# Performance work log

Measured on AMD Instinct MI355X. Metric: run time of the kernel, lower is better.

## Reference

```python
import jax, jax.numpy as jnp
import numpy as np

HEADS = 8
DIM_HEAD = 64
MAX_POS = 512
SCALE = DIM_HEAD ** -0.5

def setup_inputs() -> dict:
    key = jax.random.key(0)
    ks = jax.random.split(key, 4)
    b, n, dim = 32, 512, 512
    x = jax.random.normal(ks[0], (b, n, dim), dtype=jnp.float32)
    W_qkv = jax.random.normal(ks[1], (dim, 3 * HEADS * DIM_HEAD), dtype=jnp.float32) * (dim ** -0.5)
    rel_table = jax.random.normal(ks[2], (2 * MAX_POS + 1, DIM_HEAD), dtype=jnp.float32) * 0.02
    W_out = jax.random.normal(ks[3], (HEADS * DIM_HEAD, dim), dtype=jnp.float32) * ((HEADS * DIM_HEAD) ** -0.5)
    b_out = jnp.zeros((dim,), dtype=jnp.float32)
    return {"x": x, "W_qkv": W_qkv, "rel_table": rel_table, "W_out": W_out, "b_out": b_out}

def reference(x, W_qkv, rel_table, W_out, b_out):
    b, n, dim = x.shape
    qkv = x @ W_qkv  # [b, n, 3*h*d]
    q, k, v = jnp.split(qkv, 3, axis=-1)
    def heads(t):  # [b, n, h*d] -> [b, h, n, d]
        return t.reshape(b, n, HEADS, DIM_HEAD).transpose(0, 2, 1, 3)
    q, k, v = heads(q), heads(k), heads(v)
    dots = jnp.einsum('bhid,bhjd->bhij', q, k) * SCALE
    # relative position bias
    seq = jnp.arange(n)
    dist = jnp.clip(seq[:, None] - seq[None, :], -MAX_POS, MAX_POS) + MAX_POS  # [n, n]
    rel = rel_table[dist]  # [n, n(=r), d]
    pos_attn = jnp.einsum('bhnd,nrd->bhnr', q, rel) * SCALE
    dots = dots + pos_attn
    attn = jax.nn.softmax(dots.astype(jnp.float32), axis=-1).astype(q.dtype)
    out = jnp.einsum('bhij,bhjd->bhid', attn, v)  # [b, h, n, d]
    out = out.transpose(0, 2, 1, 3).reshape(b, n, HEADS * DIM_HEAD)
    return out @ W_out + b_out  # dropout=0.0 -> identity
```

## Files before the change

kernel.cpp:

```cpp
#include <hip/hip_runtime.h>

typedef __attribute__((ext_vector_type(8))) short short8;
typedef __attribute__((ext_vector_type(4))) float floatx4;

static constexpr size_t QOFF = 0;
static constexpr size_t KOFF = 8388608;
static constexpr size_t VTOFF = 16777216;
static constexpr size_t RBOFF = 25165824;
static constexpr size_t XBOFF = 25231424;
static constexpr size_t WTOFF = 33620032;
static constexpr size_t WOTOFF = 34406464;
static constexpr size_t OBOFF = 34668608;

__device__ inline unsigned short f2b(float f) {
  unsigned int u = __float_as_uint(f);
  u += 0x7fffu + ((u >> 16) & 1u);
  return (unsigned short)(u >> 16);
}
__device__ inline float b2f(unsigned short h) {
  return __uint_as_float(((unsigned int)h) << 16);
}

__global__ void rel_cvt(const float* __restrict__ rel, unsigned short* __restrict__ dst) {
  int i = blockIdx.x * 256 + threadIdx.x;
  if (i < 65600) dst[i] = f2b(rel[i]);
}

__global__ __launch_bounds__(256) void x_cvt(const float* __restrict__ in,
                                             unsigned short* __restrict__ dst) {
  size_t i8 = ((size_t)blockIdx.x * 256 + threadIdx.x) * 8;
  float4 a = *(const float4*)(in + i8);
  float4 b = *(const float4*)(in + i8 + 4);
  unsigned short t[8] = {f2b(a.x), f2b(a.y), f2b(a.z), f2b(a.w),
                         f2b(b.x), f2b(b.y), f2b(b.z), f2b(b.w)};
  *(uint4*)(dst + i8) = *(uint4*)t;
}

__global__ __launch_bounds__(256) void t_cvt(const float* __restrict__ in,
                                             unsigned short* __restrict__ out,
                                             int R, int C) {
  __shared__ float T[64 * 65];
  const int tid = threadIdx.x;
  const int c0 = blockIdx.x * 64, r0 = blockIdx.y * 64;
#pragma unroll
  for (int p = 0; p < 4; ++p) {
    int r = (tid >> 4) + p * 16, c4 = (tid & 15) * 4;
    float4 v = *(const float4*)(in + (size_t)(r0 + r) * C + c0 + c4);
    T[r * 65 + c4 + 0] = v.x;
    T[r * 65 + c4 + 1] = v.y;
    T[r * 65 + c4 + 2] = v.z;
    T[r * 65 + c4 + 3] = v.w;
  }
  __syncthreads();
#pragma unroll
  for (int p = 0; p < 4; ++p) {
    int oc = (tid >> 4) + p * 16;
    int or4 = (tid & 15) * 4;
    unsigned short t[4];
#pragma unroll
    for (int j = 0; j < 4; ++j) t[j] = f2b(T[(or4 + j) * 65 + oc]);
    *(uint2*)(out + (size_t)(c0 + oc) * R + r0 + or4) = *(uint2*)t;
  }
}

__global__ __launch_bounds__(256) void qkv_mfma(const unsigned short* __restrict__ Xb,
                                                const unsigned short* __restrict__ Wt,
                                                unsigned short* __restrict__ wsb) {
  __shared__ __align__(16) unsigned short As[128 * 40];
  __shared__ __align__(16) unsigned short Bs[128 * 40];
  const int tid = threadIdx.x;
  const int w = tid >> 6, lane = tid & 63;
  const int g = lane >> 4, c = lane & 15;
  const int m0 = blockIdx.x * 128, n0 = blockIdx.y * 128;
  const int wr = (w >> 1) * 64, wc = (w & 1) * 64;
  const bool vmode = (blockIdx.y >= 8);

  floatx4 acc[4][4];
#pragma unroll
  for (int mi = 0; mi < 4; ++mi)
#pragma unroll
    for (int ni = 0; ni < 4; ++ni) acc[mi][ni] = (floatx4){0.f, 0.f, 0.f, 0.f};

  for (int kk = 0; kk < 512; kk += 32) {
    __syncthreads();
#pragma unroll
    for (int p = 0; p < 2; ++p) {
      int e = tid + 256 * p;
      int r = e >> 2, o = e & 3;
      *(uint4*)(As + r * 40 + o * 8) = *(const uint4*)(Xb + (size_t)(m0 + r) * 512 + kk + o * 8);
      *(uint4*)(Bs + r * 40 + o * 8) = *(const uint4*)(Wt + (size_t)(n0 + r) * 512 + kk + o * 8);
    }
    __syncthreads();
    short8 a[4], b[4];
#pragma unroll
    for (int mi = 0; mi < 4; ++mi) a[mi] = *(const short8*)(As + (wr + mi * 16 + c) * 40 + g * 8);
#pragma unroll
    for (int ni = 0; ni < 4; ++ni) b[ni] = *(const short8*)(Bs + (wc + ni * 16 + c) * 40 + g * 8);
    if (vmode) {
#pragma unroll
      for (int mi = 0; mi < 4; ++mi)
#pragma unroll
        for (int ni = 0; ni < 4; ++ni)
          acc[mi][ni] = __builtin_amdgcn_mfma_f32_16x16x32_bf16(b[ni], a[mi], acc[mi][ni], 0, 0, 0);
    } else {
#pragma unroll
      for (int mi = 0; mi < 4; ++mi)
#pragma unroll
        for (int ni = 0; ni < 4; ++ni)
          acc[mi][ni] = __builtin_amdgcn_mfma_f32_16x16x32_bf16(a[mi], b[ni], acc[mi][ni], 0, 0, 0);
    }
  }

  constexpr float SCL = 0.125f * 1.44269504088896340736f;
  if (vmode) {
#pragma unroll
    for (int mi = 0; mi < 4; ++mi) {
      const int xrow = m0 + wr + mi * 16 + c;
      const int bb = xrow >> 9, nn = xrow & 511;
#pragma unroll
      for (int ni = 0; ni < 4; ++ni) {
#pragma unroll
        for (int r = 0; r < 4; ++r) {
          const int C = n0 + wc + ni * 16 + g * 4 + r;
          const int col512 = C & 511;
          const int h = col512 >> 6, d = col512 & 63;
          wsb[VTOFF + (size_t)(bb * 8 + h) * 32768 + (size_t)d * 512 + nn] = f2b(acc[mi][ni][r]);
        }
      }
    }
  } else {
    const size_t base = (blockIdx.y >= 4) ? KOFF : QOFF;
    const float scl = (blockIdx.y >= 4) ? 1.0f : SCL;
#pragma unroll
    for (int ni = 0; ni < 4; ++ni) {
      const int C = n0 + wc + ni * 16 + c;
      const int col512 = C & 511;
      const int h = col512 >> 6, d = col512 & 63;
#pragma unroll
      for (int mi = 0; mi < 4; ++mi) {
#pragma unroll
        for (int r = 0; r < 4; ++r) {
          const int xrow = m0 + wr + mi * 16 + g * 4 + r;
          wsb[base + (size_t)((xrow >> 9) * 8 + h) * 32768 + (size_t)(xrow & 511) * 64 + d] =
              f2b(acc[mi][ni][r] * scl);
        }
      }
    }
  }
}

__global__ __launch_bounds__(256) void attn_mfma(const unsigned short* __restrict__ wsb,
                                                 unsigned short* __restrict__ Ob) {
  __shared__ __align__(16) unsigned short Qs[64 * 72];
  __shared__ __align__(16) unsigned short Ks[64 * 72];
  __shared__ __align__(16) unsigned short Vt[64 * 72];
  __shared__ __align__(16) unsigned short Ts[128 * 72];
  __shared__ __align__(16) unsigned short Gs[64 * 136];
  __shared__ __align__(16) unsigned short Ps[64 * 72];

  const int tid = threadIdx.x;
  const int w = tid >> 6, lane = tid & 63;
  const int g = lane >> 4, c = lane & 15;
  const int i0 = blockIdx.x * 64, bh = blockIdx.y;

  const unsigned short* Qg = wsb + QOFF + (size_t)bh * 32768 + (size_t)i0 * 64;
  const unsigned short* Kg = wsb + KOFF + (size_t)bh * 32768;
  const unsigned short* Vg = wsb + VTOFF + (size_t)bh * 32768;
  const unsigned short* Rg = wsb + RBOFF;

  for (int e = tid; e < 512; e += 256) {
    int r = e >> 3, o = e & 7;
    *(uint4*)(Qs + r * 72 + o * 8) = *(const uint4*)(Qg + r * 64 + o * 8);
  }

  float m_i[4] = {-1e30f, -1e30f, -1e30f, -1e30f};
  float l_i[4] = {0.f, 0.f, 0.f, 0.f};
  floatx4 oa[4];
#pragma unroll
  for (int t = 0; t < 4; ++t) oa[t] = (floatx4){0.f, 0.f, 0.f, 0.f};

  for (int jc = 0; jc < 8; ++jc) {
    const int j0 = jc * 64;
    __syncthreads();
    for (int e = tid; e < 512; e += 256) {
      int r = e >> 3, o = e & 7;
      *(uint4*)(Ks + r * 72 + o * 8) = *(const uint4*)(Kg + (size_t)(j0 + r) * 64 + o * 8);
      *(uint4*)(Vt + r * 72 + o * 8) = *(const uint4*)(Vg + (size_t)r * 512 + j0 + o * 8);
    }
    const int dbase = i0 - j0 + 449;
    for (int e = tid; e < 1024; e += 256) {
      int r = e >> 3, o = e & 7;
      *(uint4*)(Ts + r * 72 + o * 8) = *(const uint4*)(Rg + (size_t)(dbase + r) * 64 + o * 8);
    }
    __syncthreads();

    const int arow = (w * 16 + c) * 72;
    short8 aq0 = *(const short8*)(Qs + arow + g * 8);
    short8 aq1 = *(const short8*)(Qs + arow + 32 + g * 8);

#pragma unroll
    for (int dt = 0; dt < 8; ++dt) {
      floatx4 ga = (floatx4){0.f, 0.f, 0.f, 0.f};
      short8 bt0 = *(const short8*)(Ts + (dt * 16 + c) * 72 + g * 8);
      short8 bt1 = *(const short8*)(Ts + (dt * 16 + c) * 72 + 32 + g * 8);
      ga = __builtin_amdgcn_mfma_f32_16x16x32_bf16(aq0, bt0, ga, 0, 0, 0);
      ga = __builtin_amdgcn_mfma_f32_16x16x32_bf16(aq1, bt1, ga, 0, 0, 0);
#pragma unroll
      for (int r = 0; r < 4; ++r)
        Gs[(w * 16 + g * 4 + r) * 136 + dt * 16 + c] = f2b(ga[r]);
    }

    floatx4 s4[4];
#pragma unroll
    for (int t = 0; t < 4; ++t) {
      floatx4 sa = (floatx4){0.f, 0.f, 0.f, 0.f};
      short8 bk0 = *(const short8*)(Ks + (t * 16 + c) * 72 + g * 8);
      short8 bk1 = *(const short8*)(Ks + (t * 16 + c) * 72 + 32 + g * 8);
      sa = __builtin_amdgcn_mfma_f32_16x16x32_bf16(aq0, bk0, sa, 0, 0, 0);
      sa = __builtin_amdgcn_mfma_f32_16x16x32_bf16(aq1, bk1, sa, 0, 0, 0);
      s4[t] = sa;
    }
#pragma unroll
    for (int t = 0; t < 4; ++t) {
      const int jj = t * 16 + c;
#pragma unroll
      for (int r = 0; r < 4; ++r) {
        const int il = w * 16 + g * 4 + r;
        s4[t][r] += b2f(Gs[il * 136 + (il - jj + 63)]);
      }
    }

#pragma unroll
    for (int r = 0; r < 4; ++r) {
      float mx = fmaxf(fmaxf(s4[0][r], s4[1][r]), fmaxf(s4[2][r], s4[3][r]));
#pragma unroll
      for (int msk = 1; msk < 16; msk <<= 1) mx = fmaxf(mx, __shfl_xor(mx, msk));
      const float mn = fmaxf(m_i[r], mx);
      const float al = exp2f(m_i[r] - mn);
      m_i[r] = mn;
      float ls = 0.f;
#pragma unroll
      for (int t = 0; t < 4; ++t) {
        float p = exp2f(s4[t][r] - mn);
        s4[t][r] = p;
        ls += p;
      }
#pragma unroll
      for (int msk = 1; msk < 16; msk <<= 1) ls += __shfl_xor(ls, msk);
      l_i[r] = l_i[r] * al + ls;
#pragma unroll
      for (int dt = 0; dt < 4; ++dt) oa[dt][r] *= al;
#pragma unroll
      for (int t = 0; t < 4; ++t)
        Ps[(w * 16 + g * 4 + r) * 72 + t * 16 + c] = f2b(s4[t][r]);
    }

#pragma unroll
    for (int s = 0; s < 2; ++s) {
      short8 ap = *(const short8*)(Ps + arow + s * 32 + g * 8);
#pragma unroll
      for (int dt = 0; dt < 4; ++dt) {
        short8 bv = *(const short8*)(Vt + (dt * 16 + c) * 72 + s * 32 + g * 8);
        oa[dt] = __builtin_amdgcn_mfma_f32_16x16x32_bf16(ap, bv, oa[dt], 0, 0, 0);
      }
    }
  }

  const int b = bh >> 3, h = bh & 7;
#pragma unroll
  for (int r = 0; r < 4; ++r) {
    const float inv = 1.0f / l_i[r];
    const int i = i0 + w * 16 + g * 4 + r;
    const size_t rowoff = ((size_t)(b * 512 + i)) * 512 + h * 64;
#pragma unroll
    for (int dt = 0; dt < 4; ++dt) Ob[rowoff + dt * 16 + c] = f2b(oa[dt][r] * inv);
  }
}

__global__ __launch_bounds__(256) void out_mfma(const unsigned short* __restrict__ Ab,
                                                const unsigned short* __restrict__ Bt,
                                                const float* __restrict__ bias,
                                                float* __restrict__ out) {
  __shared__ __align__(16) unsigned short As[128 * 40];
  __shared__ __align__(16) unsigned short Bs[128 * 40];
  const int tid = threadIdx.x;
  const int w = tid >> 6, lane = tid & 63;
  const int g = lane >> 4, c = lane & 15;
  const int m0 = blockIdx.x * 128, n0 = blockIdx.y * 128;
  const int wr = (w >> 1) * 64, wc = (w & 1) * 64;

  floatx4 acc[4][4];
#pragma unroll
  for (int mi = 0; mi < 4; ++mi)
#pragma unroll
    for (int ni = 0; ni < 4; ++ni) acc[mi][ni] = (floatx4){0.f, 0.f, 0.f, 0.f};

  for (int kk = 0; kk < 512; kk += 32) {
    __syncthreads();
#pragma unroll
    for (int p = 0; p < 2; ++p) {
      int e = tid + 256 * p;
      int r = e >> 2, o = e & 3;
      *(uint4*)(As + r * 40 + o * 8) = *(const uint4*)(Ab + (size_t)(m0 + r) * 512 + kk + o * 8);
      *(uint4*)(Bs + r * 40 + o * 8) = *(const uint4*)(Bt + (size_t)(n0 + r) * 512 + kk + o * 8);
    }
    __syncthreads();
    short8 a[4], b[4];
#pragma unroll
    for (int mi = 0; mi < 4; ++mi) a[mi] = *(const short8*)(As + (wr + mi * 16 + c) * 40 + g * 8);
#pragma unroll
    for (int ni = 0; ni < 4; ++ni) b[ni] = *(const short8*)(Bs + (wc + ni * 16 + c) * 40 + g * 8);
#pragma unroll
    for (int mi = 0; mi < 4; ++mi)
#pragma unroll
      for (int ni = 0; ni < 4; ++ni)
        acc[mi][ni] = __builtin_amdgcn_mfma_f32_16x16x32_bf16(a[mi], b[ni], acc[mi][ni], 0, 0, 0);
  }

#pragma unroll
  for (int ni = 0; ni < 4; ++ni) {
    const int C = n0 + wc + ni * 16 + c;
    const float bv = bias[C];
#pragma unroll
    for (int mi = 0; mi < 4; ++mi) {
#pragma unroll
      for (int r = 0; r < 4; ++r) {
        const int m = m0 + wr + mi * 16 + g * 4 + r;
        out[(size_t)m * 512 + C] = acc[mi][ni][r] + bv;
      }
    }
  }
}

extern "C" void kernel_launch(void* const* d_in, const int* in_sizes, int n_in,
                              void* d_out, int out_size, void* d_ws, size_t ws_size,
                              hipStream_t stream) {
  const float* x = (const float*)d_in[0];
  const float* Wqkv = (const float*)d_in[1];
  const float* rel = (const float*)d_in[2];
  const float* Wout = (const float*)d_in[3];
  const float* bout = (const float*)d_in[4];
  float* out = (float*)d_out;
  unsigned short* wsb = (unsigned short*)d_ws;

  rel_cvt<<<257, 256, 0, stream>>>(rel, wsb + RBOFF);
  x_cvt<<<4096, 256, 0, stream>>>(x, wsb + XBOFF);
  t_cvt<<<dim3(24, 8), 256, 0, stream>>>(Wqkv, wsb + WTOFF, 512, 1536);
  t_cvt<<<dim3(8, 8), 256, 0, stream>>>(Wout, wsb + WOTOFF, 512, 512);
  qkv_mfma<<<dim3(128, 12), 256, 0, stream>>>(wsb + XBOFF, wsb + WTOFF, wsb);
  attn_mfma<<<dim3(8, 256), 256, 0, stream>>>(wsb, wsb + OBOFF);
  out_mfma<<<dim3(128, 4), 256, 0, stream>>>(wsb + OBOFF, wsb + WOTOFF, bout, out);
}
```

Measured before the change: 305.2 us.

## Transpose attention MFMA so query is the B operand and softmax is per-lane

Puts the query fragments straight into registers as the B operand of the MFMA and computes S^T, so each lane owns one query row. The row max and sum then need only two cross-group shuffles instead of per-row 16-lane reductions. The relative-position bias tiles are read straight from global memory. Only the 6 needed 16-row diagonal blocks are computed, and they are stored per wave in fp32 in shared memory instead of a bf16 block-wide buffer. This cuts shared-memory footprint and traffic for Q and T, and drops a bf16 rounding of the bias, at the cost of uncached global loads and extra shuffles to broadcast the rescale factors.

```diff
diff --git a/kernel.cpp b/kernel.cpp
--- a/kernel.cpp
+++ b/kernel.cpp
@@ -16,9 +16,6 @@
   unsigned int u = __float_as_uint(f);
   u += 0x7fffu + ((u >> 16) & 1u);
   return (unsigned short)(u >> 16);
-}
-__device__ inline float b2f(unsigned short h) {
-  return __uint_as_float(((unsigned int)h) << 16);
 }
 
 __global__ void rel_cvt(const float* __restrict__ rel, unsigned short* __restrict__ dst) {
@@ -151,12 +148,10 @@
 
 __global__ __launch_bounds__(256) void attn_mfma(const unsigned short* __restrict__ wsb,
                                                  unsigned short* __restrict__ Ob) {
-  __shared__ __align__(16) unsigned short Qs[64 * 72];
   __shared__ __align__(16) unsigned short Ks[64 * 72];
   __shared__ __align__(16) unsigned short Vt[64 * 72];
-  __shared__ __align__(16) unsigned short Ts[128 * 72];
-  __shared__ __align__(16) unsigned short Gs[64 * 136];
   __shared__ __align__(16) unsigned short Ps[64 * 72];
+  __shared__ __align__(16) float Gs[4 * 16 * 100];
 
   const int tid = threadIdx.x;
   const int w = tid >> 6, lane = tid & 63;
@@ -168,13 +163,13 @@
   const unsigned short* Vg = wsb + VTOFF + (size_t)bh * 32768;
   const unsigned short* Rg = wsb + RBOFF;
 
-  for (int e = tid; e < 512; e += 256) {
-    int r = e >> 3, o = e & 7;
-    *(uint4*)(Qs + r * 72 + o * 8) = *(const uint4*)(Qg + r * 64 + o * 8);
-  }
-
-  float m_i[4] = {-1e30f, -1e30f, -1e30f, -1e30f};
-  float l_i[4] = {0.f, 0.f, 0.f, 0.f};
+  const short8 bq0 = *(const short8*)(Qg + (size_t)(w * 16 + c) * 64 + g * 8);
+  const short8 bq1 = *(const short8*)(Qg + (size_t)(w * 16 + c) * 64 + 32 + g * 8);
+
+  float* GsW = Gs + w * 1600;
+  unsigned short* PsW = Ps + (w * 16 + c) * 72;
+
+  float m_i = -1e30f, l_i = 0.f;
   floatx4 oa[4];
 #pragma unroll
   for (int t = 0; t < 4; ++t) oa[t] = (floatx4){0.f, 0.f, 0.f, 0.f};
@@ -187,90 +182,89 @@
       *(uint4*)(Ks + r * 72 + o * 8) = *(const uint4*)(Kg + (size_t)(j0 + r) * 64 + o * 8);
       *(uint4*)(Vt + r * 72 + o * 8) = *(const uint4*)(Vg + (size_t)r * 512 + j0 + o * 8);
     }
-    const int dbase = i0 - j0 + 449;
-    for (int e = tid; e < 1024; e += 256) {
-      int r = e >> 3, o = e & 7;
-      *(uint4*)(Ts + r * 72 + o * 8) = *(const uint4*)(Rg + (size_t)(dbase + r) * 64 + o * 8);
-    }
-    __syncthreads();
-
-    const int arow = (w * 16 + c) * 72;
-    short8 aq0 = *(const short8*)(Qs + arow + g * 8);
-    short8 aq1 = *(const short8*)(Qs + arow + 32 + g * 8);
-
-#pragma unroll
-    for (int dt = 0; dt < 8; ++dt) {
+    __syncthreads();
+
+    const int dbase = i0 - j0 + 449 + w * 16;
+    const unsigned short* Trow = Rg + (size_t)dbase * 64 + (size_t)c * 64;
+#pragma unroll
+    for (int dd = 0; dd < 6; ++dd) {
+      short8 t0 = *(const short8*)(Trow + dd * 1024 + g * 8);
+      short8 t1 = *(const short8*)(Trow + dd * 1024 + 32 + g * 8);
       floatx4 ga = (floatx4){0.f, 0.f, 0.f, 0.f};
-      short8 bt0 = *(const short8*)(Ts + (dt * 16 + c) * 72 + g * 8);
-      short8 bt1 = *(const short8*)(Ts + (dt * 16 + c) * 72 + 32 + g * 8);
-      ga = __builtin_amdgcn_mfma_f32_16x16x32_bf16(aq0, bt0, ga, 0, 0, 0);
-      ga = __builtin_amdgcn_mfma_f32_16x16x32_bf16(aq1, bt1, ga, 0, 0, 0);
-#pragma unroll
-      for (int r = 0; r < 4; ++r)
-        Gs[(w * 16 + g * 4 + r) * 136 + dt * 16 + c] = f2b(ga[r]);
+      ga = __builtin_amdgcn_mfma_f32_16x16x32_bf16(t0, bq0, ga, 0, 0, 0);
+      ga = __builtin_amdgcn_mfma_f32_16x16x32_bf16(t1, bq1, ga, 0, 0, 0);
+      *(floatx4*)(GsW + c * 100 + dd * 16 + 4 * g) = ga;
     }
 
     floatx4 s4[4];
 #pragma unroll
     for (int t = 0; t < 4; ++t) {
+      short8 k0 = *(const short8*)(Ks + (t * 16 + c) * 72 + g * 8);
+      short8 k1 = *(const short8*)(Ks + (t * 16 + c) * 72 + 32 + g * 8);
       floatx4 sa = (floatx4){0.f, 0.f, 0.f, 0.f};
-      short8 bk0 = *(const short8*)(Ks + (t * 16 + c) * 72 + g * 8);
-      short8 bk1 = *(const short8*)(Ks + (t * 16 + c) * 72 + 32 + g * 8);
-      sa = __builtin_amdgcn_mfma_f32_16x16x32_bf16(aq0, bk0, sa, 0, 0, 0);
-      sa = __builtin_amdgcn_mfma_f32_16x16x32_bf16(aq1, bk1, sa, 0, 0, 0);
+      sa = __builtin_amdgcn_mfma_f32_16x16x32_bf16(k0, bq0, sa, 0, 0, 0);
+      sa = __builtin_amdgcn_mfma_f32_16x16x32_bf16(k1, bq1, sa, 0, 0, 0);
       s4[t] = sa;
     }
-#pragma unroll
-    for (int t = 0; t < 4; ++t) {
-      const int jj = t * 16 + c;
+
+    const float* Grow = GsW + c * 100 + c + 63;
+#pragma unroll
+    for (int t = 0; t < 4; ++t)
+#pragma unroll
+      for (int r = 0; r < 4; ++r) s4[t][r] += Grow[-(16 * t + 4 * g + r)];
+
+    float mx = -1e30f;
+#pragma unroll
+    for (int t = 0; t < 4; ++t)
+      mx = fmaxf(mx, fmaxf(fmaxf(s4[t][0], s4[t][1]), fmaxf(s4[t][2], s4[t][3])));
+    mx = fmaxf(mx, __shfl_xor(mx, 16));
+    mx = fmaxf(mx, __shfl_xor(mx, 32));
+    const float mn = fmaxf(m_i, mx);
+    const float al = exp2f(m_i - mn);
+    m_i = mn;
+    float ls = 0.f;
+#pragma unroll
+    for (int t = 0; t < 4; ++t)
 #pragma unroll
       for (int r = 0; r < 4; ++r) {
-        const int il = w * 16 + g * 4 + r;
-        s4[t][r] += b2f(Gs[il * 136 + (il - jj + 63)]);
-      }
-    }
-
-#pragma unroll
-    for (int r = 0; r < 4; ++r) {
-      float mx = fmaxf(fmaxf(s4[0][r], s4[1][r]), fmaxf(s4[2][r], s4[3][r]));
-#pragma unroll
-      for (int msk = 1; msk < 16; msk <<= 1) mx = fmaxf(mx, __shfl_xor(mx, msk));
-      const float mn = fmaxf(m_i[r], mx);
-      const float al = exp2f(m_i[r] - mn);
-      m_i[r] = mn;
-      float ls = 0.f;
-#pragma unroll
-      for (int t = 0; t < 4; ++t) {
         float p = exp2f(s4[t][r] - mn);
         s4[t][r] = p;
         ls += p;
       }
-#pragma unroll
-      for (int msk = 1; msk < 16; msk <<= 1) ls += __shfl_xor(ls, msk);
-      l_i[r] = l_i[r] * al + ls;
-#pragma unroll
-      for (int dt = 0; dt < 4; ++dt) oa[dt][r] *= al;
-#pragma unroll
-      for (int t = 0; t < 4; ++t)
-        Ps[(w * 16 + g * 4 + r) * 72 + t * 16 + c] = f2b(s4[t][r]);
-    }
-
-#pragma unroll
-    for (int s = 0; s < 2; ++s) {
-      short8 ap = *(const short8*)(Ps + arow + s * 32 + g * 8);
-#pragma unroll
-      for (int dt = 0; dt < 4; ++dt) {
-        short8 bv = *(const short8*)(Vt + (dt * 16 + c) * 72 + s * 32 + g * 8);
-        oa[dt] = __builtin_amdgcn_mfma_f32_16x16x32_bf16(ap, bv, oa[dt], 0, 0, 0);
-      }
+    ls += __shfl_xor(ls, 16);
+    ls += __shfl_xor(ls, 32);
+    l_i = l_i * al + ls;
+
+#pragma unroll
+    for (int r = 0; r < 4; ++r) {
+      const float ar = __shfl(al, 4 * g + r);
+#pragma unroll
+      for (int dt = 0; dt < 4; ++dt) oa[dt][r] *= ar;
+    }
+
+#pragma unroll
+    for (int t = 0; t < 4; ++t) {
+      unsigned short pk[4] = {f2b(s4[t][0]), f2b(s4[t][1]), f2b(s4[t][2]), f2b(s4[t][3])};
+      *(uint2*)(PsW + t * 16 + 4 * g) = *(uint2*)pk;
+    }
+
+    short8 ap0 = *(const short8*)(PsW + g * 8);
+    short8 ap1 = *(const short8*)(PsW + 32 + g * 8);
+#pragma unroll
+    for (int dt = 0; dt < 4; ++dt) {
+      short8 bv0 = *(const short8*)(Vt + (dt * 16 + c) * 72 + g * 8);
+      short8 bv1 = *(const short8*)(Vt + (dt * 16 + c) * 72 + 32 + g * 8);
+      oa[dt] = __builtin_amdgcn_mfma_f32_16x16x32_bf16(ap0, bv0, oa[dt], 0, 0, 0);
+      oa[dt] = __builtin_amdgcn_mfma_f32_16x16x32_bf16(ap1, bv1, oa[dt], 0, 0, 0);
     }
   }
 
   const int b = bh >> 3, h = bh & 7;
+  const float invl = 1.0f / l_i;
 #pragma unroll
   for (int r = 0; r < 4; ++r) {
-    const float inv = 1.0f / l_i[r];
-    const int i = i0 + w * 16 + g * 4 + r;
+    const float inv = __shfl(invl, 4 * g + r);
+    const int i = i0 + w * 16 + 4 * g + r;
     const size_t rowoff = ((size_t)(b * 512 + i)) * 512 + h * 64;
 #pragma unroll
     for (int dt = 0; dt < 4; ++dt) Ob[rowoff + dt * 16 + c] = f2b(oa[dt][r] * inv);
```

Result: no change. 305.1 us (-0.0%).
